# Optimization experiments

Measured on AMD Instinct MI355X. Metric: run time of the kernel, lower is better.

Reference implementation:

```python
import jax, jax.numpy as jnp
import numpy as np

N, E, F_IN, ED, H, C, G, ACT = 50000, 800000, 32, 5, 2, 32, 128, 8
HC = H * C


def _glorot(key, shape):
    fan_in, fan_out = shape[0], shape[-1]
    lim = (6.0 / (fan_in + fan_out)) ** 0.5
    return jax.random.uniform(key, shape, jnp.float32, -lim, lim)


def setup_inputs() -> dict:
    key = jax.random.key(0)
    ks = jax.random.split(key, 32)
    inp = {
        "x": jax.random.normal(ks[0], (N, F_IN), jnp.float32),
        "edge_index": jax.random.randint(ks[1], (2, E), 0, N, jnp.int64),
        "edge_attr": jax.random.normal(ks[2], (E, ED), jnp.float32),
        "batch": jnp.sort(jax.random.randint(ks[3], (N,), 0, G, jnp.int64)),
    }
    ki = 4
    for l, din in zip((1, 2, 3), (F_IN, HC, HC)):
        inp[f"W{l}"] = _glorot(ks[ki], (din, HC)); ki += 1
        inp[f"We{l}"] = _glorot(ks[ki], (ED, HC)); ki += 1
        inp[f"as{l}"] = _glorot(ks[ki], (H, C)); ki += 1
        inp[f"ad{l}"] = _glorot(ks[ki], (H, C)); ki += 1
        inp[f"ae{l}"] = _glorot(ks[ki], (H, C)); ki += 1
        inp[f"b{l}"] = jnp.zeros((HC,), jnp.float32)
    inp["Wl"] = _glorot(ks[ki], (HC, ACT)); ki += 1
    inp["bl"] = jnp.zeros((ACT,), jnp.float32)
    return inp


def _add_self_loops(edge_index, edge_attr):
    # PyG add_self_loops with fill_value='mean': self-loop edge_attr at node i
    # is the mean of edge_attr of edges whose dst is i (0 if none).
    dst = edge_index[1]
    deg = jax.ops.segment_sum(jnp.ones((E,), jnp.float32), dst, num_segments=N)
    loop_attr = jax.ops.segment_sum(edge_attr, dst, num_segments=N) / jnp.clip(deg, 1.0)[:, None]
    loops = jnp.arange(N, dtype=edge_index.dtype)
    ei = jnp.concatenate([edge_index, jnp.stack([loops, loops])], axis=1)
    ea = jnp.concatenate([edge_attr, loop_attr], axis=0)
    return ei, ea


def _gat_layer(x, src, dst, ea, W, We, a_s, a_d, a_e, b):
    xs = (x @ W).reshape(N, H, C)                      # node features per head
    e = (ea @ We).reshape(-1, H, C)                    # edge features per head
    a_src = jnp.einsum('nhc,hc->nh', xs, a_s)
    a_dst = jnp.einsum('nhc,hc->nh', xs, a_d)
    a_edge = jnp.einsum('ehc,hc->eh', e, a_e)
    logits = jax.nn.leaky_relu(a_src[src] + a_dst[dst] + a_edge, 0.2)  # [E',H]
    m = jax.ops.segment_max(logits, dst, num_segments=N)
    m = jnp.where(jnp.isfinite(m), m, 0.0)
    ex = jnp.exp(logits - m[dst])
    den = jax.ops.segment_sum(ex, dst, num_segments=N)
    alpha = ex / (den[dst] + 1e-16)
    msg = xs[src] * alpha[..., None]                   # [E',H,C]
    out = jax.ops.segment_sum(msg, dst, num_segments=N).reshape(N, HC)
    return out + b


def reference(x, edge_index, edge_attr, batch,
              W1, We1, as1, ad1, ae1, b1,
              W2, We2, as2, ad2, ae2, b2,
              W3, We3, as3, ad3, ae3, b3,
              Wl, bl):
    ei, ea = _add_self_loops(edge_index, edge_attr)
    src, dst = ei[0], ei[1]
    h = jax.nn.relu(_gat_layer(x, src, dst, ea, W1, We1, as1, ad1, ae1, b1))
    h = jax.nn.relu(_gat_layer(h, src, dst, ea, W2, We2, as2, ad2, ae2, b2))
    h = _gat_layer(h, src, dst, ea, W3, We3, as3, ad3, ae3, b3)
    # global mean pool over graphs
    cnt = jax.ops.segment_sum(jnp.ones((N,), jnp.float32), batch, num_segments=G)
    pooled = jax.ops.segment_sum(h, batch, num_segments=G) / jnp.clip(cnt, 1.0)[:, None]
    return jnp.tanh(pooled @ Wl + bl)
```

## Files before the change

### kernel.cpp

```cpp
#include <hip/hip_runtime.h>
#include <math.h>

#define N_NODES 50000
#define N_EDGES 800000
#define E_DIM   5
#define N_G     128
#define N_ACT   8
#define SBLK    512
#define SNB     ((N_NODES + SBLK - 1) / SBLK)


__global__ __launch_bounds__(256) void setup_kernel(
    const int* __restrict__ ei, const int* __restrict__ batch,
    const float* __restrict__ We1, const float* __restrict__ ae1,
    const float* __restrict__ We2, const float* __restrict__ ae2,
    const float* __restrict__ We3, const float* __restrict__ ae3,
    float* __restrict__ weff, int* __restrict__ gstart, int* __restrict__ hist) {
    int bid = blockIdx.x, tid = threadIdx.x;
    if (bid == 0) {
        if (tid <= N_G) {
            int g = tid, lo = 0, hi = N_NODES;
            while (lo < hi) { int mid = (lo + hi) >> 1; if (batch[mid] < g) lo = mid + 1; else hi = mid; }
            gstart[g] = lo;
        }
        int t = tid - 160;
        if (t >= 0 && t < 30) {
            int l = t / 10, r = t % 10, d = r >> 1, h = r & 1;
            const float* We = (l == 0) ? We1 : (l == 1) ? We2 : We3;
            const float* ae = (l == 0) ? ae1 : (l == 1) ? ae2 : ae3;
            float s = 0.f;
            for (int c = 0; c < 32; ++c) s += We[d * 64 + h * 32 + c] * ae[h * 32 + c];
            weff[l * 10 + d * 2 + h] = s;
        }
        return;
    }
    int k = (bid - 1) * 256 + tid;
    if (k < N_EDGES) atomicAdd(&hist[ei[N_EDGES + k]], 1);
}

__device__ __forceinline__ int wave_incl_scan(int v, int lane) {
    #pragma unroll
    for (int off = 1; off < 64; off <<= 1) {
        int n = __shfl_up(v, off);
        if (lane >= off) v += n;
    }
    return v;
}

__global__ __launch_bounds__(SBLK) void scan_bsum_kernel(const int* __restrict__ hist,
                                                         int* __restrict__ bsum) {
    int i = blockIdx.x * SBLK + threadIdx.x;
    int v = (i < N_NODES) ? hist[i] : 0;
    __shared__ int sm[SBLK / 64];
    int lane = threadIdx.x & 63, w = threadIdx.x >> 6;
    #pragma unroll
    for (int o = 32; o; o >>= 1) v += __shfl_xor(v, o);
    if (lane == 0) sm[w] = v;
    __syncthreads();
    if (threadIdx.x == 0) {
        int s = 0;
        #pragma unroll
        for (int k = 0; k < SBLK / 64; ++k) s += sm[k];
        bsum[blockIdx.x] = s;
    }
}

__global__ __launch_bounds__(128) void scan_boffs_kernel(int* __restrict__ bsum) {
    int t = threadIdx.x;
    int v = (t < SNB) ? bsum[t] : 0;
    int lane = t & 63, w = t >> 6;
    int inc = wave_incl_scan(v, lane);
    __shared__ int wtot[2];
    if (lane == 63) wtot[w] = inc;
    __syncthreads();
    int base = (w == 1) ? wtot[0] : 0;
    if (t < SNB) bsum[t] = base + inc - v;
}

__global__ __launch_bounds__(SBLK) void scan_rowptr_kernel(const int* __restrict__ hist,
                                                           const int* __restrict__ bsum,
                                                           int* __restrict__ rowptr) {
    int i = blockIdx.x * SBLK + threadIdx.x;
    int v = (i < N_NODES) ? hist[i] : 0;
    int lane = threadIdx.x & 63, w = threadIdx.x >> 6;
    int inc = wave_incl_scan(v, lane);
    __shared__ int wtot[SBLK / 64];
    if (lane == 63) wtot[w] = inc;
    __syncthreads();
    int woff = 0;
    for (int k = 0; k < w; ++k) woff += wtot[k];
    int excl = bsum[blockIdx.x] + woff + inc - v;
    if (i < N_NODES) rowptr[i] = excl;
    if (i == N_NODES - 1) rowptr[N_NODES] = excl + v;
}

__global__ void scatter_kernel(const int* __restrict__ ei, const float* __restrict__ ea,
                               const float* __restrict__ weff,
                               const int* __restrict__ rowptr, int* __restrict__ cur,
                               float* __restrict__ rec) {
    int k = blockIdx.x * blockDim.x + threadIdx.x;
    if (k >= N_EDGES) return;
    int s = ei[k], d = ei[N_EDGES + k];
    const float* ep = ea + (size_t)k * E_DIM;
    float e[5];
    #pragma unroll
    for (int j = 0; j < 5; ++j) e[j] = ep[j];
    float r[6] = {0.f, 0.f, 0.f, 0.f, 0.f, 0.f};
    #pragma unroll
    for (int j = 0; j < 5; ++j) {
        r[0] += e[j] * weff[j * 2];      r[1] += e[j] * weff[j * 2 + 1];
        r[2] += e[j] * weff[10 + j * 2]; r[3] += e[j] * weff[10 + j * 2 + 1];
        r[4] += e[j] * weff[20 + j * 2]; r[5] += e[j] * weff[20 + j * 2 + 1];
    }
    int pos = rowptr[d] + atomicAdd(&cur[d], 1);
    float4* rp = (float4*)(rec + (size_t)pos * 8);
    rp[0] = make_float4(r[0], r[1], r[2], r[3]);
    rp[1] = make_float4(r[4], r[5], __int_as_float(s), 0.f);
}


template <int DIN>
__global__ __launch_bounds__(256) void feat_kernel(
    const float* __restrict__ in, const float* __restrict__ W,
    const float* __restrict__ a_s, const float* __restrict__ a_d,
    float* __restrict__ xs, float* __restrict__ a_srcv, float* __restrict__ a_dstv) {
    __shared__ float Wl[DIN * 64];
    __shared__ float asl[64], adl[64];
    int tid = threadIdx.x;
    {
        const float4* Wg = (const float4*)W;
        float4* Wl4 = (float4*)Wl;
        #pragma unroll
        for (int i = tid; i < DIN * 16; i += 256) Wl4[i] = Wg[i];
        if (tid < 64) { asl[tid] = a_s[tid]; adl[tid] = a_d[tid]; }
    }
    __syncthreads();
    int n = blockIdx.x * 64 + (tid >> 2);
    int strip = tid & 3;
    if (n >= N_NODES) return;
    float4 xr[DIN / 4];
    const float4* row4 = (const float4*)(in + (size_t)n * DIN);
    #pragma unroll
    for (int k4 = 0; k4 < DIN / 4; ++k4) xr[k4] = row4[k4];
    float4 acc[4];
    #pragma unroll
    for (int j = 0; j < 4; ++j) acc[j] = make_float4(0.f, 0.f, 0.f, 0.f);
    const float4* W4 = (const float4*)Wl;
    #pragma unroll
    for (int k4 = 0; k4 < DIN / 4; ++k4) {
        float xk[4] = {xr[k4].x, xr[k4].y, xr[k4].z, xr[k4].w};
        #pragma unroll
        for (int kk = 0; kk < 4; ++kk) {
            int k = k4 * 4 + kk;
            #pragma unroll
            for (int j = 0; j < 4; ++j) {
                float4 w = W4[k * 16 + strip * 4 + j];
                acc[j].x += xk[kk] * w.x; acc[j].y += xk[kk] * w.y;
                acc[j].z += xk[kk] * w.z; acc[j].w += xk[kk] * w.w;
            }
        }
    }
    float ps = 0.f, pd = 0.f;
    #pragma unroll
    for (int j = 0; j < 4; ++j) {
        int c = strip * 16 + j * 4;
        ps += acc[j].x * asl[c] + acc[j].y * asl[c + 1] + acc[j].z * asl[c + 2] + acc[j].w * asl[c + 3];
        pd += acc[j].x * adl[c] + acc[j].y * adl[c + 1] + acc[j].z * adl[c + 2] + acc[j].w * adl[c + 3];
    }
    ps += __shfl_xor(ps, 1);
    pd += __shfl_xor(pd, 1);
    if ((strip & 1) == 0) {
        int h = strip >> 1;
        a_srcv[n * 2 + h] = ps;
        a_dstv[n * 2 + h] = pd;
    }
    float4* o = (float4*)(xs + (size_t)n * 64 + strip * 16);
    #pragma unroll
    for (int j = 0; j < 4; ++j) o[j] = acc[j];
}

template <int L>
__global__ __launch_bounds__(256) void node_agg_kernel(
    const int* __restrict__ rowptr, const float* __restrict__ rec,
    const float* __restrict__ a_srcv, const float* __restrict__ a_dstv,
    const float* __restrict__ xs, const float* __restrict__ b,
    float* __restrict__ out, int relu) {
    int wid = blockIdx.x * 4 + (threadIdx.x >> 6);
    int lane = threadIdx.x & 63;
    if (wid >= N_NODES) return;
    int beg = rowptr[wid], end = rowptr[wid + 1];
    float2 ad2 = ((const float2*)a_dstv)[wid];
    int g = lane >> 4, fl = lane & 15, h = fl >> 3;
    float m0 = -INFINITY, m1 = -INFINITY;
    float4 accA = make_float4(0.f, 0.f, 0.f, 0.f);
    float4 accB = make_float4(0.f, 0.f, 0.f, 0.f);
    float denA = 0.f, denB = 0.f;
    float aes0 = 0.f, aes1 = 0.f;
    for (int cb = beg; cb < end; cb += 64) {
        int j = cb + lane;
        float l0 = -INFINITY, l1 = -INFINITY;
        int s = 0;
        if (j < end) {
            const float4* rp = (const float4*)(rec + (size_t)j * 8);
            float4 r0 = rp[0];
            float4 r1 = rp[1];
            s = __float_as_int(r1.z);
            float aex = (L == 0) ? r0.x : (L == 1) ? r0.z : r1.x;
            float aey = (L == 0) ? r0.y : (L == 1) ? r0.w : r1.y;
            aes0 += aex; aes1 += aey;
            float2 as2 = ((const float2*)a_srcv)[s];
            l0 = as2.x + ad2.x + aex;
            l1 = as2.y + ad2.y + aey;
            l0 = (l0 > 0.f) ? l0 : 0.2f * l0;
            l1 = (l1 > 0.f) ? l1 : 0.2f * l1;
        }
        float c0 = l0, c1 = l1;
        #pragma unroll
        for (int o = 32; o; o >>= 1) {
            c0 = fmaxf(c0, __shfl_xor(c0, o));
            c1 = fmaxf(c1, __shfl_xor(c1, o));
        }
        float n0 = fmaxf(m0, c0), n1 = fmaxf(m1, c1);
        float scale = h ? expf(m1 - n1) : expf(m0 - n0);
        accA.x *= scale; accA.y *= scale; accA.z *= scale; accA.w *= scale;
        accB.x *= scale; accB.y *= scale; accB.z *= scale; accB.w *= scale;
        denA *= scale; denB *= scale;
        m0 = n0; m1 = n1;
        float ex0 = expf(l0 - m0);
        float ex1 = expf(l1 - m1);
        int cnt = min(end - cb, 64);
        for (int t8 = 0; t8 < cnt; t8 += 8) {
            int tA = t8 + g;
            int tB = tA + 4;
            float e0 = __shfl(ex0, tA), e1 = __shfl(ex1, tA);
            int sA = __shfl(s, tA);
            float f0 = __shfl(ex0, tB), f1 = __shfl(ex1, tB);
            int sB = __shfl(s, tB);
            float eA = h ? e1 : e0;
            float eB = h ? f1 : f0;
            float4 xv = *(const float4*)(xs + (size_t)sA * 64 + fl * 4);
            float4 yv = *(const float4*)(xs + (size_t)sB * 64 + fl * 4);
            accA.x += eA * xv.x; accA.y += eA * xv.y; accA.z += eA * xv.z; accA.w += eA * xv.w;
            denA += eA;
            accB.x += eB * yv.x; accB.y += eB * yv.y; accB.z += eB * yv.z; accB.w += eB * yv.w;
            denB += eB;
        }
    }
    float4 acc = make_float4(accA.x + accB.x, accA.y + accB.y,
                             accA.z + accB.z, accA.w + accB.w);
    float den = denA + denB;
    #pragma unroll
    for (int o = 16; o <= 32; o <<= 1) {
        acc.x += __shfl_xor(acc.x, o); acc.y += __shfl_xor(acc.y, o);
        acc.z += __shfl_xor(acc.z, o); acc.w += __shfl_xor(acc.w, o);
        den   += __shfl_xor(den, o);
    }
    #pragma unroll
    for (int o = 1; o < 64; o <<= 1) {
        aes0 += __shfl_xor(aes0, o);
        aes1 += __shfl_xor(aes1, o);
    }
    if (lane < 16) {
        int ne = end - beg;
        float aeS = (h ? aes1 : aes0) / fmaxf((float)ne, 1.f);
        float2 as2 = ((const float2*)a_srcv)[wid];
        float ls = (h ? as2.y + ad2.y : as2.x + ad2.x) + aeS;
        ls = (ls > 0.f) ? ls : 0.2f * ls;
        float mh = h ? m1 : m0;
        float nm = fmaxf(mh, ls);
        float sc = expf(mh - nm);
        float exS = expf(ls - nm);
        den = den * sc + exS;
        float4 xv = *(const float4*)(xs + (size_t)wid * 64 + fl * 4);
        float inv = 1.f / (den + 1e-16f);
        float4 b4 = ((const float4*)b)[fl];
        float4 v;
        v.x = (acc.x * sc + exS * xv.x) * inv + b4.x;
        v.y = (acc.y * sc + exS * xv.y) * inv + b4.y;
        v.z = (acc.z * sc + exS * xv.z) * inv + b4.z;
        v.w = (acc.w * sc + exS * xv.w) * inv + b4.w;
        if (relu) {
            v.x = fmaxf(v.x, 0.f); v.y = fmaxf(v.y, 0.f);
            v.z = fmaxf(v.z, 0.f); v.w = fmaxf(v.w, 0.f);
        }
        ((float4*)(out + (size_t)wid * 64))[fl] = v;
    }
}


__global__ __launch_bounds__(256) void pool_kernel(const float* __restrict__ hfeat,
                                                   const int* __restrict__ gstart,
                                                   float* __restrict__ pooled) {
    __shared__ float sm[4][64];
    int g = blockIdx.x;
    int w = threadIdx.x >> 6, lane = threadIdx.x & 63;
    int beg = gstart[g], end = gstart[g + 1];
    float acc = 0.f;
    for (int n = beg + w; n < end; n += 4)
        acc += hfeat[(size_t)n * 64 + lane];
    sm[w][lane] = acc;
    __syncthreads();
    if (w == 0) {
        float v = sm[0][lane] + sm[1][lane] + sm[2][lane] + sm[3][lane];
        pooled[g * 64 + lane] = v / fmaxf((float)(end - beg), 1.f);
    }
}

__global__ void head_kernel(const float* __restrict__ pooled,
                            const float* __restrict__ Wl, const float* __restrict__ bl,
                            float* __restrict__ out) {
    int t = blockIdx.x * blockDim.x + threadIdx.x;
    if (t >= N_G * N_ACT) return;
    int g = t >> 3, a = t & 7;
    float s = bl[a];
    #pragma unroll
    for (int j = 0; j < 64; ++j) s += pooled[g * 64 + j] * Wl[j * 8 + a];
    out[t] = tanhf(s);
}

extern "C" void kernel_launch(void* const* d_in, const int* in_sizes, int n_in,
                              void* d_out, int out_size, void* d_ws, size_t ws_size,
                              hipStream_t stream) {
    const float* x    = (const float*)d_in[0];
    const int*   ei   = (const int*)d_in[1];
    const float* ea   = (const float*)d_in[2];
    const int*   batch= (const int*)d_in[3];
    const float* W[3]   = {(const float*)d_in[4],  (const float*)d_in[10], (const float*)d_in[16]};
    const float* We[3]  = {(const float*)d_in[5],  (const float*)d_in[11], (const float*)d_in[17]};
    const float* as_[3] = {(const float*)d_in[6],  (const float*)d_in[12], (const float*)d_in[18]};
    const float* ad_[3] = {(const float*)d_in[7],  (const float*)d_in[13], (const float*)d_in[19]};
    const float* ae_[3] = {(const float*)d_in[8],  (const float*)d_in[14], (const float*)d_in[20]};
    const float* b_[3]  = {(const float*)d_in[9],  (const float*)d_in[15], (const float*)d_in[21]};
    const float* Wlin = (const float*)d_in[22];
    const float* bl   = (const float*)d_in[23];
    float* out = (float*)d_out;

    float* ws = (float*)d_ws;
    size_t off = 0;
    float* A      = ws + off; off += (size_t)N_NODES * 64;
    float* B      = ws + off; off += (size_t)N_NODES * 64;
    float* rec    = ws + off; off += (size_t)N_EDGES * 8;
    float* a_srcv = ws + off; off += N_NODES * 2;
    float* a_dstv = ws + off; off += N_NODES * 2;
    float* weff   = ws + off; off += 32;
    float* pooled = ws + off; off += N_G * 64;
    int* rowptr = (int*)(ws + off); off += N_NODES + 1;
    int* hist   = (int*)(ws + off); off += N_NODES;
    int* cur    = (int*)(ws + off); off += N_NODES;
    int* gstart = (int*)(ws + off); off += N_G + 1;
    int* bsum   = (int*)(ws + off); off += SNB;

    hipMemsetAsync(hist, 0, 2 * N_NODES * sizeof(int), stream);
    setup_kernel<<<1 + (N_EDGES + 255) / 256, 256, 0, stream>>>(
        ei, batch, We[0], ae_[0], We[1], ae_[1], We[2], ae_[2], weff, gstart, hist);
    scan_bsum_kernel<<<SNB, SBLK, 0, stream>>>(hist, bsum);
    scan_boffs_kernel<<<1, 128, 0, stream>>>(bsum);
    scan_rowptr_kernel<<<SNB, SBLK, 0, stream>>>(hist, bsum, rowptr);
    scatter_kernel<<<(N_EDGES + 255) / 256, 256, 0, stream>>>(ei, ea, weff, rowptr, cur, rec);

    const int NB = (N_NODES + 3) / 4;
    const int FB = (N_NODES + 63) / 64;
    for (int l = 0; l < 3; ++l) {
        if (l == 0)
            feat_kernel<32><<<FB, 256, 0, stream>>>(x, W[0], as_[0], ad_[0], B, a_srcv, a_dstv);
        else
            feat_kernel<64><<<FB, 256, 0, stream>>>(A, W[l], as_[l], ad_[l], B, a_srcv, a_dstv);
        if (l == 0)
            node_agg_kernel<0><<<NB, 256, 0, stream>>>(rowptr, rec, a_srcv, a_dstv, B, b_[0], A, 1);
        else if (l == 1)
            node_agg_kernel<1><<<NB, 256, 0, stream>>>(rowptr, rec, a_srcv, a_dstv, B, b_[1], A, 1);
        else
            node_agg_kernel<2><<<NB, 256, 0, stream>>>(rowptr, rec, a_srcv, a_dstv, B, b_[2], A, 0);
    }
    pool_kernel<<<N_G, 256, 0, stream>>>(A, gstart, pooled);
    head_kernel<<<(N_G * N_ACT + 255) / 256, 256, 0, stream>>>(pooled, Wlin, bl, out);
}
```

Measured before the change: 390.0 us.

## Use 16-lane groups per node in aggregation, two-pass CSR build, fuse pool/head and scan

The node aggregation kernel now gives each destination node 16 lanes instead of a full 64-lane wavefront, so four nodes share a wave, and it unrolls four neighbor gathers per step. This targets idle lanes, since the average degree is about 16. The edge scatter is split into two passes: a coalesced write of edge records plus a permutation index, then a gather into CSR order, replacing scattered 32-byte writes. The block-offset scan kernel is folded into the rowptr kernel, and the pool and head kernels are merged to save launches.

```diff
diff --git a/kernel.cpp b/kernel.cpp
--- a/kernel.cpp
+++ b/kernel.cpp
@@ -65,39 +65,36 @@
     }
 }
 
-__global__ __launch_bounds__(128) void scan_boffs_kernel(int* __restrict__ bsum) {
-    int t = threadIdx.x;
-    int v = (t < SNB) ? bsum[t] : 0;
-    int lane = t & 63, w = t >> 6;
-    int inc = wave_incl_scan(v, lane);
-    __shared__ int wtot[2];
-    if (lane == 63) wtot[w] = inc;
-    __syncthreads();
-    int base = (w == 1) ? wtot[0] : 0;
-    if (t < SNB) bsum[t] = base + inc - v;
-}
-
 __global__ __launch_bounds__(SBLK) void scan_rowptr_kernel(const int* __restrict__ hist,
                                                            const int* __restrict__ bsum,
                                                            int* __restrict__ rowptr) {
-    int i = blockIdx.x * SBLK + threadIdx.x;
+    __shared__ int s_boffs;
+    __shared__ int wtot[SBLK / 64];
+    int bid = blockIdx.x;
+    if (threadIdx.x < 64) {
+        int v = 0;
+        for (int i = threadIdx.x; i < bid; i += 64) v += bsum[i];
+        #pragma unroll
+        for (int o = 32; o; o >>= 1) v += __shfl_xor(v, o);
+        if (threadIdx.x == 0) s_boffs = v;
+    }
+    int i = bid * SBLK + threadIdx.x;
     int v = (i < N_NODES) ? hist[i] : 0;
     int lane = threadIdx.x & 63, w = threadIdx.x >> 6;
     int inc = wave_incl_scan(v, lane);
-    __shared__ int wtot[SBLK / 64];
     if (lane == 63) wtot[w] = inc;
     __syncthreads();
     int woff = 0;
     for (int k = 0; k < w; ++k) woff += wtot[k];
-    int excl = bsum[blockIdx.x] + woff + inc - v;
+    int excl = s_boffs + woff + inc - v;
     if (i < N_NODES) rowptr[i] = excl;
     if (i == N_NODES - 1) rowptr[N_NODES] = excl + v;
 }
 
-__global__ void scatter_kernel(const int* __restrict__ ei, const float* __restrict__ ea,
-                               const float* __restrict__ weff,
-                               const int* __restrict__ rowptr, int* __restrict__ cur,
-                               float* __restrict__ rec) {
+__global__ void scatterA_kernel(const int* __restrict__ ei, const float* __restrict__ ea,
+                                const float* __restrict__ weff,
+                                const int* __restrict__ rowptr, int* __restrict__ cur,
+                                float* __restrict__ recE, int* __restrict__ iperm) {
     int k = blockIdx.x * blockDim.x + threadIdx.x;
     if (k >= N_EDGES) return;
     int s = ei[k], d = ei[N_EDGES + k];
@@ -112,10 +109,24 @@
         r[2] += e[j] * weff[10 + j * 2]; r[3] += e[j] * weff[10 + j * 2 + 1];
         r[4] += e[j] * weff[20 + j * 2]; r[5] += e[j] * weff[20 + j * 2 + 1];
     }
-    int pos = rowptr[d] + atomicAdd(&cur[d], 1);
-    float4* rp = (float4*)(rec + (size_t)pos * 8);
+    float4* rp = (float4*)(recE + (size_t)k * 8);
     rp[0] = make_float4(r[0], r[1], r[2], r[3]);
     rp[1] = make_float4(r[4], r[5], __int_as_float(s), 0.f);
+    int pos = rowptr[d] + atomicAdd(&cur[d], 1);
+    iperm[pos] = k;
+}
+
+__global__ void gatherB_kernel(const int* __restrict__ iperm, const float* __restrict__ recE,
+                               float* __restrict__ rec) {
+    int pos = blockIdx.x * blockDim.x + threadIdx.x;
+    if (pos >= N_EDGES) return;
+    int k = iperm[pos];
+    const float4* sp = (const float4*)(recE + (size_t)k * 8);
+    float4 r0 = sp[0];
+    float4 r1 = sp[1];
+    float4* dp = (float4*)(rec + (size_t)pos * 8);
+    dp[0] = r0;
+    dp[1] = r1;
 }
 
 
@@ -185,19 +196,19 @@
     const float* __restrict__ a_srcv, const float* __restrict__ a_dstv,
     const float* __restrict__ xs, const float* __restrict__ b,
     float* __restrict__ out, int relu) {
-    int wid = blockIdx.x * 4 + (threadIdx.x >> 6);
+    int nid = (blockIdx.x * 256 + threadIdx.x) >> 4;
+    if (nid >= N_NODES) return;
     int lane = threadIdx.x & 63;
-    if (wid >= N_NODES) return;
-    int beg = rowptr[wid], end = rowptr[wid + 1];
-    float2 ad2 = ((const float2*)a_dstv)[wid];
-    int g = lane >> 4, fl = lane & 15, h = fl >> 3;
+    int fl = lane & 15, h = fl >> 3;
+    int gbase = lane & 48;
+    int beg = rowptr[nid], end = rowptr[nid + 1];
+    float2 ad2 = ((const float2*)a_dstv)[nid];
     float m0 = -INFINITY, m1 = -INFINITY;
-    float4 accA = make_float4(0.f, 0.f, 0.f, 0.f);
-    float4 accB = make_float4(0.f, 0.f, 0.f, 0.f);
-    float denA = 0.f, denB = 0.f;
+    float4 acc = make_float4(0.f, 0.f, 0.f, 0.f);
+    float den0 = 0.f, den1 = 0.f;
     float aes0 = 0.f, aes1 = 0.f;
-    for (int cb = beg; cb < end; cb += 64) {
-        int j = cb + lane;
+    for (int cb = beg; cb < end; cb += 16) {
+        int j = cb + fl;
         float l0 = -INFINITY, l1 = -INFINITY;
         int s = 0;
         if (j < end) {
@@ -216,82 +227,75 @@
         }
         float c0 = l0, c1 = l1;
         #pragma unroll
-        for (int o = 32; o; o >>= 1) {
+        for (int o = 8; o; o >>= 1) {
             c0 = fmaxf(c0, __shfl_xor(c0, o));
             c1 = fmaxf(c1, __shfl_xor(c1, o));
         }
         float n0 = fmaxf(m0, c0), n1 = fmaxf(m1, c1);
-        float scale = h ? expf(m1 - n1) : expf(m0 - n0);
-        accA.x *= scale; accA.y *= scale; accA.z *= scale; accA.w *= scale;
-        accB.x *= scale; accB.y *= scale; accB.z *= scale; accB.w *= scale;
-        denA *= scale; denB *= scale;
+        float sc0 = expf(m0 - n0), sc1 = expf(m1 - n1);
+        den0 *= sc0; den1 *= sc1;
+        float sa = h ? sc1 : sc0;
+        acc.x *= sa; acc.y *= sa; acc.z *= sa; acc.w *= sa;
         m0 = n0; m1 = n1;
         float ex0 = expf(l0 - m0);
         float ex1 = expf(l1 - m1);
-        int cnt = min(end - cb, 64);
-        for (int t8 = 0; t8 < cnt; t8 += 8) {
-            int tA = t8 + g;
-            int tB = tA + 4;
-            float e0 = __shfl(ex0, tA), e1 = __shfl(ex1, tA);
-            int sA = __shfl(s, tA);
-            float f0 = __shfl(ex0, tB), f1 = __shfl(ex1, tB);
-            int sB = __shfl(s, tB);
-            float eA = h ? e1 : e0;
-            float eB = h ? f1 : f0;
-            float4 xv = *(const float4*)(xs + (size_t)sA * 64 + fl * 4);
-            float4 yv = *(const float4*)(xs + (size_t)sB * 64 + fl * 4);
-            accA.x += eA * xv.x; accA.y += eA * xv.y; accA.z += eA * xv.z; accA.w += eA * xv.w;
-            denA += eA;
-            accB.x += eB * yv.x; accB.y += eB * yv.y; accB.z += eB * yv.z; accB.w += eB * yv.w;
-            denB += eB;
-        }
-    }
-    float4 acc = make_float4(accA.x + accB.x, accA.y + accB.y,
-                             accA.z + accB.z, accA.w + accB.w);
-    float den = denA + denB;
-    #pragma unroll
-    for (int o = 16; o <= 32; o <<= 1) {
-        acc.x += __shfl_xor(acc.x, o); acc.y += __shfl_xor(acc.y, o);
-        acc.z += __shfl_xor(acc.z, o); acc.w += __shfl_xor(acc.w, o);
-        den   += __shfl_xor(den, o);
-    }
-    #pragma unroll
-    for (int o = 1; o < 64; o <<= 1) {
-        aes0 += __shfl_xor(aes0, o);
-        aes1 += __shfl_xor(aes1, o);
-    }
-    if (lane < 16) {
-        int ne = end - beg;
-        float aeS = (h ? aes1 : aes0) / fmaxf((float)ne, 1.f);
-        float2 as2 = ((const float2*)a_srcv)[wid];
-        float ls = (h ? as2.y + ad2.y : as2.x + ad2.x) + aeS;
-        ls = (ls > 0.f) ? ls : 0.2f * ls;
-        float mh = h ? m1 : m0;
-        float nm = fmaxf(mh, ls);
-        float sc = expf(mh - nm);
-        float exS = expf(ls - nm);
-        den = den * sc + exS;
-        float4 xv = *(const float4*)(xs + (size_t)wid * 64 + fl * 4);
-        float inv = 1.f / (den + 1e-16f);
-        float4 b4 = ((const float4*)b)[fl];
-        float4 v;
-        v.x = (acc.x * sc + exS * xv.x) * inv + b4.x;
-        v.y = (acc.y * sc + exS * xv.y) * inv + b4.y;
-        v.z = (acc.z * sc + exS * xv.z) * inv + b4.z;
-        v.w = (acc.w * sc + exS * xv.w) * inv + b4.w;
-        if (relu) {
-            v.x = fmaxf(v.x, 0.f); v.y = fmaxf(v.y, 0.f);
-            v.z = fmaxf(v.z, 0.f); v.w = fmaxf(v.w, 0.f);
-        }
-        ((float4*)(out + (size_t)wid * 64))[fl] = v;
-    }
-}
-
-
-__global__ __launch_bounds__(256) void pool_kernel(const float* __restrict__ hfeat,
-                                                   const int* __restrict__ gstart,
-                                                   float* __restrict__ pooled) {
+        den0 += ex0; den1 += ex1;
+        int cnt = min(end - cb, 16);
+        for (int t4 = 0; t4 < cnt; t4 += 4) {
+            int tA = gbase + t4;
+            float eA0 = __shfl(ex0, tA),     eA1 = __shfl(ex1, tA);     int sA = __shfl(s, tA);
+            float eB0 = __shfl(ex0, tA + 1), eB1 = __shfl(ex1, tA + 1); int sB = __shfl(s, tA + 1);
+            float eC0 = __shfl(ex0, tA + 2), eC1 = __shfl(ex1, tA + 2); int sC = __shfl(s, tA + 2);
+            float eD0 = __shfl(ex0, tA + 3), eD1 = __shfl(ex1, tA + 3); int sD = __shfl(s, tA + 3);
+            float eA = h ? eA1 : eA0, eB = h ? eB1 : eB0;
+            float eC = h ? eC1 : eC0, eD = h ? eD1 : eD0;
+            float4 xa = *(const float4*)(xs + (size_t)sA * 64 + fl * 4);
+            float4 xb = *(const float4*)(xs + (size_t)sB * 64 + fl * 4);
+            float4 xc = *(const float4*)(xs + (size_t)sC * 64 + fl * 4);
+            float4 xd = *(const float4*)(xs + (size_t)sD * 64 + fl * 4);
+            acc.x += eA * xa.x + eB * xb.x + eC * xc.x + eD * xd.x;
+            acc.y += eA * xa.y + eB * xb.y + eC * xc.y + eD * xd.y;
+            acc.z += eA * xa.z + eB * xb.z + eC * xc.z + eD * xd.z;
+            acc.w += eA * xa.w + eB * xb.w + eC * xc.w + eD * xd.w;
+        }
+    }
+    #pragma unroll
+    for (int o = 8; o; o >>= 1) {
+        den0 += __shfl_xor(den0, o); den1 += __shfl_xor(den1, o);
+        aes0 += __shfl_xor(aes0, o); aes1 += __shfl_xor(aes1, o);
+    }
+    int ne = end - beg;
+    float aeS = (h ? aes1 : aes0) / fmaxf((float)ne, 1.f);
+    float2 as2 = ((const float2*)a_srcv)[nid];
+    float ls = (h ? as2.y + ad2.y : as2.x + ad2.x) + aeS;
+    ls = (ls > 0.f) ? ls : 0.2f * ls;
+    float mh = h ? m1 : m0;
+    float nm = fmaxf(mh, ls);
+    float sc = expf(mh - nm);
+    float exS = expf(ls - nm);
+    float den = (h ? den1 : den0) * sc + exS;
+    float4 xv = *(const float4*)(xs + (size_t)nid * 64 + fl * 4);
+    float inv = 1.f / (den + 1e-16f);
+    float4 b4 = ((const float4*)b)[fl];
+    float4 v;
+    v.x = (acc.x * sc + exS * xv.x) * inv + b4.x;
+    v.y = (acc.y * sc + exS * xv.y) * inv + b4.y;
+    v.z = (acc.z * sc + exS * xv.z) * inv + b4.z;
+    v.w = (acc.w * sc + exS * xv.w) * inv + b4.w;
+    if (relu) {
+        v.x = fmaxf(v.x, 0.f); v.y = fmaxf(v.y, 0.f);
+        v.z = fmaxf(v.z, 0.f); v.w = fmaxf(v.w, 0.f);
+    }
+    ((float4*)(out + (size_t)nid * 64))[fl] = v;
+}
+
+
+__global__ __launch_bounds__(256) void pool_head_kernel(
+    const float* __restrict__ hfeat, const int* __restrict__ gstart,
+    const float* __restrict__ Wl, const float* __restrict__ bl,
+    float* __restrict__ out) {
     __shared__ float sm[4][64];
+    __shared__ float pooledL[64];
     int g = blockIdx.x;
     int w = threadIdx.x >> 6, lane = threadIdx.x & 63;
     int beg = gstart[g], end = gstart[g + 1];
@@ -302,20 +306,16 @@
     __syncthreads();
     if (w == 0) {
         float v = sm[0][lane] + sm[1][lane] + sm[2][lane] + sm[3][lane];
-        pooled[g * 64 + lane] = v / fmaxf((float)(end - beg), 1.f);
-    }
-}
-
-__global__ void head_kernel(const float* __restrict__ pooled,
-                            const float* __restrict__ Wl, const float* __restrict__ bl,
-                            float* __restrict__ out) {
-    int t = blockIdx.x * blockDim.x + threadIdx.x;
-    if (t >= N_G * N_ACT) return;
-    int g = t >> 3, a = t & 7;
-    float s = bl[a];
-    #pragma unroll
-    for (int j = 0; j < 64; ++j) s += pooled[g * 64 + j] * Wl[j * 8 + a];
-    out[t] = tanhf(s);
+        pooledL[lane] = v / fmaxf((float)(end - beg), 1.f);
+    }
+    __syncthreads();
+    if (threadIdx.x < N_ACT) {
+        int a = threadIdx.x;
+        float s = bl[a];
+        #pragma unroll
+        for (int j = 0; j < 64; ++j) s += pooledL[j] * Wl[j * 8 + a];
+        out[g * N_ACT + a] = tanhf(s);
+    }
 }
 
 extern "C" void kernel_launch(void* const* d_in, const int* in_sizes, int n_in,
@@ -339,26 +339,28 @@
     size_t off = 0;
     float* A      = ws + off; off += (size_t)N_NODES * 64;
     float* B      = ws + off; off += (size_t)N_NODES * 64;
+    float* recE   = A;
     float* rec    = ws + off; off += (size_t)N_EDGES * 8;
     float* a_srcv = ws + off; off += N_NODES * 2;
     float* a_dstv = ws + off; off += N_NODES * 2;
     float* weff   = ws + off; off += 32;
-    float* pooled = ws + off; off += N_G * 64;
     int* rowptr = (int*)(ws + off); off += N_NODES + 1;
     int* hist   = (int*)(ws + off); off += N_NODES;
     int* cur    = (int*)(ws + off); off += N_NODES;
     int* gstart = (int*)(ws + off); off += N_G + 1;
     int* bsum   = (int*)(ws + off); off += SNB;
+    int* iperm  = (int*)(ws + off); off += N_EDGES;
 
     hipMemsetAsync(hist, 0, 2 * N_NODES * sizeof(int), stream);
     setup_kernel<<<1 + (N_EDGES + 255) / 256, 256, 0, stream>>>(
         ei, batch, We[0], ae_[0], We[1], ae_[1], We[2], ae_[2], weff, gstart, hist);
     scan_bsum_kernel<<<SNB, SBLK, 0, stream>>>(hist, bsum);
-    scan_boffs_kernel<<<1, 128, 0, stream>>>(bsum);
     scan_rowptr_kernel<<<SNB, SBLK, 0, stream>>>(hist, bsum, rowptr);
-    scatter_kernel<<<(N_EDGES + 255) / 256, 256, 0, stream>>>(ei, ea, weff, rowptr, cur, rec);
-
-    const int NB = (N_NODES + 3) / 4;
+    scatterA_kernel<<<(N_EDGES + 255) / 256, 256, 0, stream>>>(ei, ea, weff, rowptr, cur,
+                                                               recE, iperm);
+    gatherB_kernel<<<(N_EDGES + 255) / 256, 256, 0, stream>>>(iperm, recE, rec);
+
+    const int NB = (N_NODES * 16 + 255) / 256;
     const int FB = (N_NODES + 63) / 64;
     for (int l = 0; l < 3; ++l) {
         if (l == 0)
@@ -372,6 +374,5 @@
         else
             node_agg_kernel<2><<<NB, 256, 0, stream>>>(rowptr, rec, a_srcv, a_dstv, B, b_[2], A, 0);
     }
-    pool_kernel<<<N_G, 256, 0, stream>>>(A, gstart, pooled);
-    head_kernel<<<(N_G * N_ACT + 255) / 256, 256, 0, stream>>>(pooled, Wlin, bl, out);
-}
+    pool_head_kernel<<<N_G, 256, 0, stream>>>(A, gstart, Wlin, bl, out);
+}
```

Result: slower. 405.3 us (+3.9%).
